# Kernel tuning notes

Hardware: AMD Instinct MI355X
Metric: run time of the kernel (lower is better)

Reference implementation:

```python
import jax, jax.numpy as jnp
import numpy as np
from jax import lax

L = 2        # encoder layers
D = 256      # d_model
H = 8        # nhead
DH = D // H  # head dim
CF = 2       # compression_factor (default in CustomizedAttn)
FF = 2048    # dim_feedforward
B = 10       # batch (forced: null_k has shape (10,1,D))
HH = 40
WW = 40
T = HH * WW  # seq len = 1600
EPS = 1e-5


def setup_inputs() -> dict:
    key = jax.random.key(0)
    ks = jax.random.split(key, 16)
    f = lambda k, shp: jax.random.normal(k, shp, jnp.float32) * 0.02
    return {
        "src": jax.random.normal(ks[0], (B, D, HH, WW), jnp.float32),
        "pos_embed": jax.random.normal(ks[1], (B, D, HH, WW), jnp.float32),
        "Wq": f(ks[2], (L, D, D)),
        "Wk": f(ks[3], (L, D, D)),
        "Wv": f(ks[4], (L, D, D)),
        "Wo": f(ks[5], (L, D, D)),
        "bo": jnp.zeros((L, D), jnp.float32),
        "conv_w": f(ks[6], (L, D, D // H, CF)),  # grouped Conv1d weight [out, in/groups, k]
        "conv_b": jnp.zeros((L, D), jnp.float32),
        "null_k": f(ks[7], (L, B, 1, D)),
        "null_v": f(ks[8], (L, B, 1, D)),
        "ln1_g": jnp.ones((L, D), jnp.float32),
        "ln1_b": jnp.zeros((L, D), jnp.float32),
        "ln2_g": jnp.ones((L, D), jnp.float32),
        "ln2_b": jnp.zeros((L, D), jnp.float32),
        "W1": f(ks[9], (L, FF, D)),
        "b1": jnp.zeros((L, FF), jnp.float32),
        "W2": f(ks[10], (L, D, FF)),
        "b2": jnp.zeros((L, D), jnp.float32),
    }


def _layernorm(x, g, b):
    m = jnp.mean(x, axis=-1, keepdims=True)
    v = jnp.var(x, axis=-1, keepdims=True)
    return (x - m) * lax.rsqrt(v + EPS) * g + b


def _attn(x, pos, Wq, Wk, Wv, Wo, bo, cw, cb, nk, nv):
    # x, pos: [B, T, D]
    qk = x + pos
    q = qk @ Wq.T
    k = qk @ Wk.T
    v = x @ Wv.T
    # torch: padding = cf - t % cf -> always in [1, cf], so padding ALWAYS applied
    pad = CF - (T % CF)
    k = jnp.pad(k, ((0, 0), (pad, 0), (0, 0)))
    v = jnp.pad(v, ((0, 0), (pad, 0), (0, 0)))

    def compress(t_):  # grouped strided Conv1d over time, shared weights for k and v
        y = lax.conv_general_dilated(
            t_.transpose(0, 2, 1), cw, (CF,), "VALID",
            dimension_numbers=("NCH", "OIH", "NCH"), feature_group_count=H)
        return (y + cb[None, :, None]).transpose(0, 2, 1)

    k = jnp.concatenate([nk, compress(k)], axis=1)  # [B, Tc+10, D]
    v = jnp.concatenate([nv, compress(v)], axis=1)
    split = lambda t_: t_.reshape(B, t_.shape[1], H, DH).transpose(0, 2, 1, 3)
    qh, kh, vh = split(q), split(k), split(v)
    # NOTE: scale uses FULL d_model (d ** -0.5), faithful to the source.
    dots = jnp.einsum("bhid,bhjd->bhij", qh, kh) * (D ** -0.5)
    # NOTE: the source computes softmax(dots) but then overwrites it with
    # dropout(dots); at inference attention weights are the raw scaled dots.
    out = jnp.einsum("bhij,bhjd->bhid", dots, vh)
    out = out.transpose(0, 2, 1, 3).reshape(B, T, D)
    return out @ Wo.T + bo


def reference(src, pos_embed, Wq, Wk, Wv, Wo, bo, conv_w, conv_b, null_k, null_v,
              ln1_g, ln1_b, ln2_g, ln2_b, W1, b1, W2, b2):
    x = src.reshape(B, D, T).transpose(0, 2, 1)        # [B, T, D]
    pos = pos_embed.reshape(B, D, T).transpose(0, 2, 1)
    for l in range(L):
        a = _attn(x, pos, Wq[l], Wk[l], Wv[l], Wo[l], bo[l],
                  conv_w[l], conv_b[l], null_k[l], null_v[l])
        x = _layernorm(x + a, ln1_g[l], ln1_b[l])
        ff = jnp.maximum(x @ W1[l].T + b1[l], 0.0) @ W2[l].T + b2[l]
        x = _layernorm(x + ff, ln2_g[l], ln2_b[l])
    return x.transpose(0, 2, 1).reshape(B, D, HH, WW)
```

## Files before the change

### kernel.cpp

```cpp
#include <hip/hip_runtime.h>
#include <math.h>

typedef __attribute__((ext_vector_type(8))) short short8;
typedef __attribute__((ext_vector_type(4))) short short4v;
typedef __attribute__((ext_vector_type(4))) float f32x4;
typedef unsigned int u32;

constexpr int Bsz = 10;
constexpr int Dm  = 256;
constexpr int Hh  = 8;
constexpr int Tt  = 1600;
constexpr int FFd = 2048;
constexpr int Tkv = 802;
constexpr int JCH = 8;
constexpr size_t Fsz  = (size_t)Bsz * Tt * Dm;
constexpr size_t PAD  = 65536;
constexpr size_t KVsz = (size_t)Bsz * Tkv * Dm;
constexpr size_t FHsz = (size_t)Bsz * Tt * FFd;
constexpr size_t WBsz = 2621440;

__device__ float g_x[Fsz];
__device__ float g_qk[Fsz];
__device__ float g_t[Fsz];
__device__ float g_kc[KVsz];
__device__ float g_vc[KVsz];
__device__ float g_kvm[(size_t)Bsz * Hh * 32 * 32];
__device__ float g_kvp[(size_t)JCH * Bsz * Hh * 32 * 32];
__device__ float g_pos[Fsz];
__device__ unsigned short g_xb[Fsz + PAD];
__device__ unsigned short g_qkb[Fsz + PAD];
__device__ unsigned short g_tb[Fsz + PAD];
__device__ unsigned short g_qb[Fsz + PAD];
__device__ unsigned short g_ffh[FHsz + PAD];
__device__ unsigned short g_wb[WBsz];
__device__ unsigned short g_wo2[(size_t)Bsz * Dm * Dm];

__device__ __forceinline__ float* selbuf(int id) {
  switch (id) {
    case 0: return g_x;
    case 1: return g_qk;
    case 2: return g_t;
    case 3: return g_kc;
    case 4: return g_vc;
    default: return g_kvm;
  }
}
__device__ __forceinline__ unsigned short* selbufb(int id) {
  switch (id) {
    case 0: return g_xb;
    case 1: return g_qkb;
    case 2: return g_tb;
    case 3: return g_ffh;
    default: return g_qb;
  }
}

__device__ __forceinline__ unsigned short f2b(float x) {
  unsigned int u = __float_as_uint(x);
  u += 0x7FFFu + ((u >> 16) & 1u);
  return (unsigned short)(u >> 16);
}
__device__ __forceinline__ float b2f(unsigned short u) {
  return __uint_as_float(((unsigned int)u) << 16);
}

__global__ __launch_bounds__(256) void wconv_k(const float* src, int dstoff, int n) {
  int i = blockIdx.x * 256 + threadIdx.x;
  if (i < n) g_wb[dstoff + i] = f2b(src[i]);
}

__global__ __launch_bounds__(256) void trans_in_k(const float* in, int oid) {
  __shared__ float tile[32][33];
  const int tx = threadIdx.x & 31, ty = threadIdx.x >> 5;
  const int t0 = blockIdx.x * 32, d0 = blockIdx.y * 32, b = blockIdx.z;
  #pragma unroll
  for (int i = ty; i < 32; i += 8)
    tile[i][tx] = in[((size_t)(b * Dm + d0 + i)) * Tt + t0 + tx];
  __syncthreads();
  float* out = (oid == 0) ? g_x : g_pos;
  #pragma unroll
  for (int i = ty; i < 32; i += 8) {
    const size_t idx = ((size_t)(b * Tt + t0 + i)) * Dm + d0 + tx;
    float v = tile[tx][i];
    out[idx] = v;
    if (oid == 0) g_xb[idx] = f2b(v);
  }
}

__global__ __launch_bounds__(256) void trans_out_k(float* out) {
  __shared__ float tile[32][33];
  const int tx = threadIdx.x & 31, ty = threadIdx.x >> 5;
  const int t0 = blockIdx.x * 32, d0 = blockIdx.y * 32, b = blockIdx.z;
  #pragma unroll
  for (int i = ty; i < 32; i += 8)
    tile[i][tx] = g_x[((size_t)(b * Tt + t0 + i)) * Dm + d0 + tx];
  __syncthreads();
  #pragma unroll
  for (int i = ty; i < 32; i += 8)
    out[((size_t)(b * Dm + d0 + i)) * Tt + t0 + tx] = tile[tx][i];
}

__global__ __launch_bounds__(256) void addpos_k(int n4) {
  int i = blockIdx.x * 256 + threadIdx.x;
  if (i >= n4) return;
  float4 a = ((const float4*)g_x)[i];
  float4 p = ((const float4*)g_pos)[i];
  short4v v;
  v[0] = (short)f2b(a.x + p.x); v[1] = (short)f2b(a.y + p.y);
  v[2] = (short)f2b(a.z + p.z); v[3] = (short)f2b(a.w + p.w);
  *(short4v*)&g_qkb[(size_t)i * 4] = v;
}

template<int BN, bool DUAL, bool PERB, bool RELU, bool BIAS, bool CBF16>
__global__ __launch_bounds__(256) void gemm2_k(
    int Aid, int woff, const float* __restrict__ bias, int Cid, int C2id,
    int NB, int M, int N, int K) {
  constexpr int BM = 128, BK = 64;
  constexpr int ACH = BM * 8;
  constexpr int BCH = BN * 8;
  constexpr int NW = BN / 32;
  __shared__ short8 As8[2][ACH];
  __shared__ short8 Bs8[2][BCH];
  const int tid = threadIdx.x;
  const int lane = tid & 63, wid = tid >> 6;
  const int wr = wid >> 1, wc = wid & 1;

  const int nwg = gridDim.x;
  const int bid = blockIdx.x;
  const int q = nwg >> 3, r = nwg & 7;
  const int xcd = bid & 7, seq = bid >> 3;
  const int wgid = (xcd < r ? xcd * (q + 1) : r * (q + 1) + (xcd - r) * q) + seq;

  int m0, n0, mlim;
  const unsigned short* W16;
  if constexpr (PERB) {
    const int per = 13 * NB;
    const int b = wgid / per;
    const int rem = wgid - b * per;
    m0 = b * Tt + (rem / NB) * BM;
    n0 = (rem % NB) * BN;
    mlim = b * Tt + Tt;
    W16 = g_wo2 + (size_t)b * 65536;
  } else {
    m0 = (wgid / NB) * BM;
    n0 = (wgid % NB) * BN;
    mlim = M;
    W16 = g_wb + woff;
  }

  const unsigned short* A16 = selbufb(Aid);
  const bool second = DUAL && (n0 >= 256);
  float* Cf = selbuf(second ? C2id : Cid);
  unsigned short* C16 = selbufb(second ? C2id : Cid);
  const int gn0 = second ? n0 - 256 : n0;
  const int cstride = DUAL ? 256 : N;

  f32x4 acc[4][NW];
  #pragma unroll
  for (int m = 0; m < 4; ++m)
    #pragma unroll
    for (int n = 0; n < NW; ++n) acc[m][n] = (f32x4){0.f, 0.f, 0.f, 0.f};

  const int lkc = lane >> 4, lrc = lane & 15;

  auto stage = [&](int t, int buf) {
    const int k0 = t * BK;
    #pragma unroll
    for (int i = 0; i < ACH / 256; ++i) {
      const int c = tid + i * 256;
      const int row = c >> 3, kc = c & 7;
      const unsigned short* gs = A16 + (size_t)(m0 + row) * K + k0 +
                                 ((kc ^ (row & 7)) << 3);
      __builtin_amdgcn_global_load_lds(
          (const __attribute__((address_space(1))) u32*)gs,
          (__attribute__((address_space(3))) u32*)&As8[buf][c], 16, 0, 0);
    }
    #pragma unroll
    for (int i = 0; i < BCH / 256; ++i) {
      const int c = tid + i * 256;
      const int row = c >> 3, kc = c & 7;
      const unsigned short* gs = W16 + (size_t)(n0 + row) * K + k0 +
                                 ((kc ^ (row & 7)) << 3);
      __builtin_amdgcn_global_load_lds(
          (const __attribute__((address_space(1))) u32*)gs,
          (__attribute__((address_space(3))) u32*)&Bs8[buf][c], 16, 0, 0);
    }
  };

  const int nt = K / BK;
  stage(0, 0);
  if (nt > 1) stage(1, 1);
  for (int t = 0; t < nt; ++t) {
    const int cur = t & 1;
    if (t + 1 < nt) {
      if constexpr (BN == 64)
        asm volatile("s_waitcnt vmcnt(6)" ::: "memory");
      else
        asm volatile("s_waitcnt vmcnt(8)" ::: "memory");
    } else {
      asm volatile("s_waitcnt vmcnt(0)" ::: "memory");
    }
    __builtin_amdgcn_sched_barrier(0);
    __builtin_amdgcn_s_barrier();
    #pragma unroll
    for (int kk = 0; kk < 2; ++kk) {
      short8 af[4], bf[NW];
      #pragma unroll
      for (int m = 0; m < 4; ++m) {
        const int r2 = wr * 64 + m * 16 + lrc;
        af[m] = As8[cur][r2 * 8 + ((kk * 4 + lkc) ^ (r2 & 7))];
      }
      #pragma unroll
      for (int n = 0; n < NW; ++n) {
        const int cn = wc * (BN / 2) + n * 16 + lrc;
        bf[n] = Bs8[cur][cn * 8 + ((kk * 4 + lkc) ^ (cn & 7))];
      }
      #pragma unroll
      for (int m = 0; m < 4; ++m)
        #pragma unroll
        for (int n = 0; n < NW; ++n)
          acc[m][n] = __builtin_amdgcn_mfma_f32_16x16x32_bf16(
              af[m], bf[n], acc[m][n], 0, 0, 0);
    }
    __builtin_amdgcn_sched_barrier(0);
    __builtin_amdgcn_s_barrier();
    __builtin_amdgcn_sched_barrier(0);
    if (t + 2 < nt) stage(t + 2, cur);
  }

  constexpr int CSTR = (BN == 64) ? BN + 4 : BN;
  float* ldsC = (float*)&As8[0][0];
  {
    asm volatile("s_waitcnt vmcnt(0)" ::: "memory");
    __builtin_amdgcn_s_barrier();
    const int r0 = lkc * 4;
    #pragma unroll
    for (int m = 0; m < 4; ++m)
      #pragma unroll
      for (int n = 0; n < NW; ++n) {
        const int col = wc * (BN / 2) + n * 16 + lrc;
        #pragma unroll
        for (int j = 0; j < 4; ++j)
          ldsC[(wr * 64 + m * 16 + r0 + j) * CSTR + col] = acc[m][n][j];
      }
    __syncthreads();
  }
  if constexpr (CBF16) {
    constexpr int CH = BM * BN / 8;
    #pragma unroll
    for (int i = 0; i < CH / 256; ++i) {
      const int c = tid + i * 256;
      const int rowl = c / (BN / 8), col8 = (c % (BN / 8)) * 8;
      if (PERB && m0 + rowl >= mlim) continue;
      short8 v;
      #pragma unroll
      for (int j = 0; j < 8; ++j) {
        float x = ldsC[rowl * CSTR + col8 + j];
        if (BIAS) x += bias[gn0 + col8 + j];
        if (RELU) x = fmaxf(x, 0.f);
        v[j] = (short)f2b(x);
      }
      *(short8*)(C16 + (size_t)(m0 + rowl) * cstride + gn0 + col8) = v;
    }
  } else {
    constexpr int CH = BM * BN / 4;
    #pragma unroll
    for (int i = 0; i < CH / 256; ++i) {
      const int c = tid + i * 256;
      const int rowl = c / (BN / 4), col4 = (c % (BN / 4)) * 4;
      if (PERB && m0 + rowl >= mlim) continue;
      float4 v;
      float* pv = &v.x;
      #pragma unroll
      for (int j = 0; j < 4; ++j) {
        float x = ldsC[rowl * CSTR + col4 + j];
        if (BIAS) x += bias[gn0 + col4 + j];
        if (RELU) x = fmaxf(x, 0.f);
        pv[j] = x;
      }
      *(float4*)(Cf + (size_t)(m0 + rowl) * cstride + gn0 + col4) = v;
    }
  }
}

template<bool RELU, bool BIAS, bool CBF16>
__global__ __launch_bounds__(512, 4) void gemmh_k(
    int Aid, int woff, const float* __restrict__ bias, int Cid,
    int NB, int M, int N) {
  constexpr int BM = 128, BN = 128, K = 256, KH = 128;
  __shared__ short8 As8[BM * 16];
  __shared__ short8 Bs8[BN * 16];
  const int tid = threadIdx.x;
  const int lane = tid & 63, wid = tid >> 6;
  const int wr = wid >> 2, wc = wid & 3;
  const int nwg = gridDim.x;
  const int bid = blockIdx.x;
  const int q = nwg >> 3, r = nwg & 7;
  const int xcd = bid & 7, seq = bid >> 3;
  const int wgid = (xcd < r ? xcd * (q + 1) : r * (q + 1) + (xcd - r) * q) + seq;
  const int m0 = (wgid / NB) * BM, n0 = (wgid % NB) * BN;
  const unsigned short* A16 = selbufb(Aid);
  const unsigned short* W16 = g_wb + woff;
  float* Cf = selbuf(Cid);
  unsigned short* C16 = selbufb(Cid);
  const int lkc = lane >> 4, lrc = lane & 15;

  f32x4 acc[4][2];
  #pragma unroll
  for (int m = 0; m < 4; ++m)
    #pragma unroll
    for (int n = 0; n < 2; ++n) acc[m][n] = (f32x4){0.f, 0.f, 0.f, 0.f};

  #pragma unroll
  for (int h = 0; h < 2; ++h) {
    const int k0 = h * KH;
    if (h) __builtin_amdgcn_s_barrier();
    #pragma unroll
    for (int i = 0; i < (BM * 16) / 512; ++i) {
      const int c = tid + i * 512;
      const int row = c >> 4, kc = c & 15;
      const unsigned short* gs = A16 + (size_t)(m0 + row) * K + k0 +
                                 ((kc ^ (row & 15)) << 3);
      __builtin_amdgcn_global_load_lds(
          (const __attribute__((address_space(1))) u32*)gs,
          (__attribute__((address_space(3))) u32*)&As8[c], 16, 0, 0);
    }
    #pragma unroll
    for (int i = 0; i < (BN * 16) / 512; ++i) {
      const int c = tid + i * 512;
      const int row = c >> 4, kc = c & 15;
      const unsigned short* gs = W16 + (size_t)(n0 + row) * K + k0 +
                                 ((kc ^ (row & 15)) << 3);
      __builtin_amdgcn_global_load_lds(
          (const __attribute__((address_space(1))) u32*)gs,
          (__attribute__((address_space(3))) u32*)&Bs8[c], 16, 0, 0);
    }
    asm volatile("s_waitcnt vmcnt(0)" ::: "memory");
    __builtin_amdgcn_sched_barrier(0);
    __builtin_amdgcn_s_barrier();

    __builtin_amdgcn_s_setprio(1);
    #pragma unroll
    for (int s = 0; s < 4; ++s) {
      short8 af[4], bf[2];
      #pragma unroll
      for (int m = 0; m < 4; ++m) {
        const int r2 = wr * 64 + m * 16 + lrc;
        af[m] = As8[r2 * 16 + ((s * 4 + lkc) ^ (r2 & 15))];
      }
      #pragma unroll
      for (int n = 0; n < 2; ++n) {
        const int cn = wc * 32 + n * 16 + lrc;
        bf[n] = Bs8[cn * 16 + ((s * 4 + lkc) ^ (cn & 15))];
      }
      #pragma unroll
      for (int m = 0; m < 4; ++m)
        #pragma unroll
        for (int n = 0; n < 2; ++n)
          acc[m][n] = __builtin_amdgcn_mfma_f32_16x16x32_bf16(
              af[m], bf[n], acc[m][n], 0, 0, 0);
    }
    __builtin_amdgcn_s_setprio(0);
  }

  const int r0 = lkc * 4;
  #pragma unroll
  for (int m = 0; m < 4; ++m) {
    const int gmb = m0 + wr * 64 + m * 16 + r0;
    #pragma unroll
    for (int n = 0; n < 2; ++n) {
      const int gn = n0 + wc * 32 + n * 16 + lrc;
      const float bb = BIAS ? bias[gn] : 0.f;
      #pragma unroll
      for (int j = 0; j < 4; ++j) {
        float v = acc[m][n][j] + bb;
        if (RELU) v = fmaxf(v, 0.f);
        if (CBF16) C16[(size_t)(gmb + j) * N + gn] = f2b(v);
        else       Cf[(size_t)(gmb + j) * N + gn] = v;
      }
    }
  }
}

__global__ __launch_bounds__(256) void compress_main_k(
    const float* __restrict__ cw, const float* __restrict__ cb,
    const float* __restrict__ nul, int out_id) {
  __shared__ float rows[32][256];
  const int tc0 = 1 + blockIdx.x * 16;
  const int b = blockIdx.y;
  const int tid = threadIdx.x;
  const int o = tid;
  const int g = o >> 5;

  const int r0g = 2 * tc0 - 2;
  const unsigned short* src = g_tb + ((size_t)b * Tt + r0g) * Dm;
  #pragma unroll
  for (int i = 0; i < 4; ++i) {
    const int c = tid + i * 256;
    const int row = c >> 5, off = (c & 31) * 8;
    short8 v = *(const short8*)(src + (size_t)row * 256 + off);
    #pragma unroll
    for (int j = 0; j < 8; ++j)
      rows[row][off + j] = b2f((unsigned short)v[j]);
  }

  float we[32], wo[32];
  {
    const float4* wp = (const float4*)(cw + o * 64);
    #pragma unroll
    for (int i = 0; i < 16; ++i) {
      float4 w4 = wp[i];
      we[i * 2 + 0] = w4.x; wo[i * 2 + 0] = w4.y;
      we[i * 2 + 1] = w4.z; wo[i * 2 + 1] = w4.w;
    }
  }
  const float bias = cb[o];
  float* outb = selbuf(out_id) + (size_t)b * Tkv * Dm;
  if (blockIdx.x == 0) {
    outb[o] = nul[b * Dm + o];
    outb[Dm + o] = bias;
  }
  __syncthreads();

  float* outp = outb + o;
  #pragma unroll
  for (int t = 0; t < 16; ++t) {
    const int lr = 2 * t;
    const float* p0 = &rows[lr][g * 32];
    const float* p1 = &rows[lr + 1][g * 32];
    float acc = bias;
    #pragma unroll
    for (int i4 = 0; i4 < 8; ++i4) {
      float4 a0 = *(const float4*)(p0 + i4 * 4);
      float4 a1 = *(const float4*)(p1 + i4 * 4);
      acc = fmaf(we[i4 * 4 + 0], a0.x, acc);
      acc = fmaf(we[i4 * 4 + 1], a0.y, acc);
      acc = fmaf(we[i4 * 4 + 2], a0.z, acc);
      acc = fmaf(we[i4 * 4 + 3], a0.w, acc);
      acc = fmaf(wo[i4 * 4 + 0], a1.x, acc);
      acc = fmaf(wo[i4 * 4 + 1], a1.y, acc);
      acc = fmaf(wo[i4 * 4 + 2], a1.z, acc);
      acc = fmaf(wo[i4 * 4 + 3], a1.w, acc);
    }
    outp[(size_t)(1 + tc0 + t) * Dm] = acc;
  }
}

__global__ __launch_bounds__(256) void kvout1_k() {
  __shared__ float kl[8][32];
  __shared__ float vl[8][32];
  const int bh = blockIdx.x;
  const int js = blockIdx.y;
  const int b = bh >> 3, h = bh & 7;
  const int j0 = js * 101;
  const int jend = (j0 + 101 < Tkv) ? j0 + 101 : Tkv;

  const int tid = threadIdx.x;
  const int lr = tid >> 5;
  const int lc = tid & 31;
  const int e = tid >> 3;
  const int d0 = (tid & 7) * 4;

  float a0 = 0.f, a1 = 0.f, a2 = 0.f, a3 = 0.f;
  const size_t base = (size_t)b * Tkv * Dm + h * 32;

  for (int jc = j0; jc < jend; jc += 8) {
    const int jr = jc + lr;
    if (jr < jend) {
      kl[lr][lc] = g_kc[base + (size_t)jr * Dm + lc];
      vl[lr][lc] = g_vc[base + (size_t)jr * Dm + lc];
    } else {
      kl[lr][lc] = 0.f;
      vl[lr][lc] = 0.f;
    }
    __syncthreads();
    #pragma unroll
    for (int r = 0; r < 8; ++r) {
      const float kf = kl[r][e];
      const float* vr = &vl[r][d0];
      a0 = fmaf(kf, vr[0], a0);
      a1 = fmaf(kf, vr[1], a1);
      a2 = fmaf(kf, vr[2], a2);
      a3 = fmaf(kf, vr[3], a3);
    }
    __syncthreads();
  }
  float* op = g_kvp + ((size_t)js * 80 + bh) * 1024 + e * 32 + d0;
  op[0] = a0; op[1] = a1; op[2] = a2; op[3] = a3;
}

__global__ __launch_bounds__(256) void kvout2_k() {
  const int bh = blockIdx.x;
  const int tid = threadIdx.x;
  const int e = tid >> 3;
  const int d0 = (tid & 7) * 4;
  float a0 = 0.f, a1 = 0.f, a2 = 0.f, a3 = 0.f;
  #pragma unroll
  for (int s = 0; s < JCH; ++s) {
    const float* p = g_kvp + ((size_t)s * 80 + bh) * 1024 + e * 32 + d0;
    a0 += p[0]; a1 += p[1]; a2 += p[2]; a3 += p[3];
  }
  float* op = g_kvm + (size_t)bh * 1024 + e * 32 + d0;
  op[0] = a0 * 0.0625f;
  op[1] = a1 * 0.0625f;
  op[2] = a2 * 0.0625f;
  op[3] = a3 * 0.0625f;
}

__global__ __launch_bounds__(256) void wo2_k(int wooff) {
  const int n = blockIdx.x, b = blockIdx.y;
  const int he = threadIdx.x;
  const int h = he >> 5, e = he & 31;
  const float* kp = g_kvm + ((size_t)(b * Hh + h) * 32 + e) * 32;
  const unsigned short* wp = g_wb + wooff + (size_t)n * Dm + h * 32;
  float acc = 0.f;
  #pragma unroll
  for (int d = 0; d < 32; ++d) acc = fmaf(kp[d], b2f(wp[d]), acc);
  g_wo2[(size_t)b * 65536 + (size_t)n * Dm + he] = f2b(acc);
}

__global__ __launch_bounds__(256) void ln_k(int did, const float* g,
                                            const float* beta, int do_pos) {
  const int lane = threadIdx.x & 63;
  const int wave = threadIdx.x >> 6;
  const size_t row = (size_t)blockIdx.x * 4 + wave;
  float4 xv = ((const float4*)g_x)[row * 64 + lane];
  float4 dv = ((const float4*)selbuf(did))[row * 64 + lane];
  float v[4] = {xv.x + dv.x, xv.y + dv.y, xv.z + dv.z, xv.w + dv.w};
  float sum = v[0] + v[1] + v[2] + v[3];
  float sq = v[0]*v[0] + v[1]*v[1] + v[2]*v[2] + v[3]*v[3];
  #pragma unroll
  for (int off = 32; off; off >>= 1) {
    sum += __shfl_xor(sum, off);
    sq  += __shfl_xor(sq, off);
  }
  const float mean = sum * (1.f / 256.f);
  const float var = sq * (1.f / 256.f) - mean * mean;
  const float rs = rsqrtf(var + 1e-5f);
  float4 gg = ((const float4*)g)[lane];
  float4 bb = ((const float4*)beta)[lane];
  float4 ov;
  ov.x = (v[0] - mean) * rs * gg.x + bb.x;
  ov.y = (v[1] - mean) * rs * gg.y + bb.y;
  ov.z = (v[2] - mean) * rs * gg.z + bb.z;
  ov.w = (v[3] - mean) * rs * gg.w + bb.w;
  ((float4*)g_x)[row * 64 + lane] = ov;
  short4v sv;
  sv[0] = (short)f2b(ov.x); sv[1] = (short)f2b(ov.y);
  sv[2] = (short)f2b(ov.z); sv[3] = (short)f2b(ov.w);
  *(short4v*)&g_xb[(row * 64 + lane) * 4] = sv;
  if (do_pos) {
    float4 pv = ((const float4*)g_pos)[row * 64 + lane];
    short4v qv;
    qv[0] = (short)f2b(ov.x + pv.x); qv[1] = (short)f2b(ov.y + pv.y);
    qv[2] = (short)f2b(ov.z + pv.z); qv[3] = (short)f2b(ov.w + pv.w);
    *(short4v*)&g_qkb[(row * 64 + lane) * 4] = qv;
  }
}

extern "C" void kernel_launch(void* const* d_in, const int* in_sizes, int n_in,
                              void* d_out, int out_size, void* d_ws, size_t ws_size,
                              hipStream_t stream) {
  const float* src  = (const float*)d_in[0];
  const float* pose = (const float*)d_in[1];
  const float* Wq   = (const float*)d_in[2];
  const float* Wk   = (const float*)d_in[3];
  const float* Wv   = (const float*)d_in[4];
  const float* Wo   = (const float*)d_in[5];
  const float* bo   = (const float*)d_in[6];
  const float* cw   = (const float*)d_in[7];
  const float* cb   = (const float*)d_in[8];
  const float* nk   = (const float*)d_in[9];
  const float* nv   = (const float*)d_in[10];
  const float* ln1g = (const float*)d_in[11];
  const float* ln1b = (const float*)d_in[12];
  const float* ln2g = (const float*)d_in[13];
  const float* ln2b = (const float*)d_in[14];
  const float* W1   = (const float*)d_in[15];
  const float* b1   = (const float*)d_in[16];
  const float* W2   = (const float*)d_in[17];
  const float* b2   = (const float*)d_in[18];

  const int MT = Bsz * Tt;
  const int NF = (int)Fsz;
  const dim3 tgrid(Tt / 32, Dm / 32, Bsz);

  const int OV = 262144, OO = 393216, O1 = 524288, O2 = 1572864;
  for (int l = 0; l < 2; ++l) {
    wconv_k<<<256, 256, 0, stream>>>(Wk + (size_t)l * 65536, l * 131072, 65536);
    wconv_k<<<256, 256, 0, stream>>>(Wq + (size_t)l * 65536, l * 131072 + 65536, 65536);
    wconv_k<<<256, 256, 0, stream>>>(Wv + (size_t)l * 65536, OV + l * 65536, 65536);
    wconv_k<<<256, 256, 0, stream>>>(Wo + (size_t)l * 65536, OO + l * 65536, 65536);
  }
  wconv_k<<<4096, 256, 0, stream>>>(W1, O1, 1048576);
  wconv_k<<<4096, 256, 0, stream>>>(W2, O2, 1048576);

  trans_in_k<<<tgrid, 256, 0, stream>>>(src, 0);
  trans_in_k<<<tgrid, 256, 0, stream>>>(pose, 7);

  const int MB = MT / 128;
  for (int l = 0; l < 2; ++l) {
    const float* bo_l = bo + (size_t)l * Dm;
    const float* cw_l = cw + (size_t)l * Dm * 64;
    const float* cb_l = cb + (size_t)l * Dm;
    const float* nk_l = nk + (size_t)l * Bsz * Dm;
    const float* nv_l = nv + (size_t)l * Bsz * Dm;
    const float* b1_l = b1 + (size_t)l * FFd;
    const float* b2_l = b2 + (size_t)l * Dm;
    const int wkq = l * 131072;
    const int wv = OV + l * 65536, wo = OO + l * 65536;
    const int w1 = O1 + l * 524288, w2 = O2 + l * 524288;

    if (l == 0) addpos_k<<<NF / 4 / 256, 256, 0, stream>>>(NF / 4);
    gemm2_k<64, true, false, false, false, true><<<8 * MB, 256, 0, stream>>>(
        1, wkq, nullptr, 2, 4, 8, MT, 512, Dm);
    compress_main_k<<<dim3(50, Bsz), 256, 0, stream>>>(cw_l, cb_l, nk_l, 3);
    gemm2_k<64, false, false, false, false, true><<<4 * MB, 256, 0, stream>>>(
        0, wv, nullptr, 2, 2, 4, MT, Dm, Dm);
    compress_main_k<<<dim3(50, Bsz), 256, 0, stream>>>(cw_l, cb_l, nv_l, 4);
    kvout1_k<<<dim3(Bsz * Hh, JCH), 256, 0, stream>>>();
    kvout2_k<<<Bsz * Hh, 256, 0, stream>>>();
    wo2_k<<<dim3(Dm, Bsz), 256, 0, stream>>>(wo);
    gemm2_k<64, false, true, false, true, false><<<Bsz * 13 * 4, 256, 0, stream>>>(
        4, 0, bo_l, 2, 2, 4, MT, Dm, Dm);
    ln_k<<<MT / 4, 256, 0, stream>>>(2, ln1g + l * Dm, ln1b + l * Dm, 0);

    gemmh_k<true, true, true><<<16 * MB, 512, 0, stream>>>(
        0, w1, b1_l, 3, 16, MT, FFd);
    gemm2_k<64, false, false, false, true, false><<<4 * MB, 256, 0, stream>>>(
        3, w2, b2_l, 1, 1, 4, MT, Dm, FFd);
    ln_k<<<MT / 4, 256, 0, stream>>>(1, ln2g + l * Dm, ln2b + l * Dm,
                                     l == 0 ? 1 : 0);
  }

  trans_out_k<<<tgrid, 256, 0, stream>>>((float*)d_out);
}
```

Before: 409.4 us.

## Fuse setup kernels, merge compress launches, add split-K W2 GEMM

Merges the ten weight-conversion launches into one kernel, fuses the two input transposes with the pos-add and bf16 casts, and batches the K and V compression into a single launch by writing V to a separate buffer. The W2 feed-forward GEMM is replaced by a new split-K kernel with a 128x256 tile. It writes its two partial sums to separate buffers, and the following layernorm now reads and adds both. This is meant to cut launch overhead and improve occupancy on the K=2048 GEMM, at the cost of an extra fp32 partial buffer round-trip through memory.

New measurement: 385.2 us. 1.06x faster.

```diff
diff --git a/kernel.cpp b/kernel.cpp
--- a/kernel.cpp
+++ b/kernel.cpp
@@ -64,26 +64,48 @@
   return __uint_as_float(((unsigned int)u) << 16);
 }
 
-__global__ __launch_bounds__(256) void wconv_k(const float* src, int dstoff, int n) {
-  int i = blockIdx.x * 256 + threadIdx.x;
-  if (i < n) g_wb[dstoff + i] = f2b(src[i]);
-}
-
-__global__ __launch_bounds__(256) void trans_in_k(const float* in, int oid) {
-  __shared__ float tile[32][33];
+__global__ __launch_bounds__(256) void wconv_all_k(
+    const float* __restrict__ Wk, const float* __restrict__ Wq,
+    const float* __restrict__ Wv, const float* __restrict__ Wo,
+    const float* __restrict__ W1, const float* __restrict__ W2) {
+  const int i = blockIdx.x * 256 + threadIdx.x;
+  float v;
+  if (i < 262144) {
+    const int l = i >> 17, r = i & 131071;
+    v = (r < 65536) ? Wk[l * 65536 + r] : Wq[l * 65536 + (r - 65536)];
+  } else if (i < 393216) {
+    v = Wv[i - 262144];
+  } else if (i < 524288) {
+    v = Wo[i - 393216];
+  } else if (i < 1572864) {
+    v = W1[i - 524288];
+  } else {
+    v = W2[i - 1572864];
+  }
+  g_wb[i] = f2b(v);
+}
+
+__global__ __launch_bounds__(256) void trans_in2_k(const float* __restrict__ src,
+                                                   const float* __restrict__ pose) {
+  __shared__ float ts[32][33];
+  __shared__ float tp[32][33];
   const int tx = threadIdx.x & 31, ty = threadIdx.x >> 5;
   const int t0 = blockIdx.x * 32, d0 = blockIdx.y * 32, b = blockIdx.z;
   #pragma unroll
-  for (int i = ty; i < 32; i += 8)
-    tile[i][tx] = in[((size_t)(b * Dm + d0 + i)) * Tt + t0 + tx];
+  for (int i = ty; i < 32; i += 8) {
+    const size_t gi = ((size_t)(b * Dm + d0 + i)) * Tt + t0 + tx;
+    ts[i][tx] = src[gi];
+    tp[i][tx] = pose[gi];
+  }
   __syncthreads();
-  float* out = (oid == 0) ? g_x : g_pos;
   #pragma unroll
   for (int i = ty; i < 32; i += 8) {
     const size_t idx = ((size_t)(b * Tt + t0 + i)) * Dm + d0 + tx;
-    float v = tile[tx][i];
-    out[idx] = v;
-    if (oid == 0) g_xb[idx] = f2b(v);
+    const float s = ts[tx][i], p = tp[tx][i];
+    g_x[idx] = s;
+    g_pos[idx] = p;
+    g_xb[idx] = f2b(s);
+    g_qkb[idx] = f2b(s + p);
   }
 }
 
@@ -98,17 +120,6 @@
   #pragma unroll
   for (int i = ty; i < 32; i += 8)
     out[((size_t)(b * Dm + d0 + i)) * Tt + t0 + tx] = tile[tx][i];
-}
-
-__global__ __launch_bounds__(256) void addpos_k(int n4) {
-  int i = blockIdx.x * 256 + threadIdx.x;
-  if (i >= n4) return;
-  float4 a = ((const float4*)g_x)[i];
-  float4 p = ((const float4*)g_pos)[i];
-  short4v v;
-  v[0] = (short)f2b(a.x + p.x); v[1] = (short)f2b(a.y + p.y);
-  v[2] = (short)f2b(a.z + p.z); v[3] = (short)f2b(a.w + p.w);
-  *(short4v*)&g_qkb[(size_t)i * 4] = v;
 }
 
 template<int BN, bool DUAL, bool PERB, bool RELU, bool BIAS, bool CBF16>
@@ -279,6 +290,110 @@
         pv[j] = x;
       }
       *(float4*)(Cf + (size_t)(m0 + rowl) * cstride + gn0 + col4) = v;
+    }
+  }
+}
+
+__global__ __launch_bounds__(512, 2) void gemmn_k(
+    int Aid, int woff, const float* __restrict__ bias, int K) {
+  constexpr int BM = 128, BN = 256, BK = 64;
+  constexpr int ACH = BM * 8;
+  constexpr int BCH = BN * 8;
+  __shared__ short8 As8[2][ACH];
+  __shared__ short8 Bs8[2][BCH];
+  const int tid = threadIdx.x;
+  const int lane = tid & 63, wid = tid >> 6;
+  const int wr = wid >> 2, wc = wid & 3;
+  const int nwg = gridDim.x, bid = blockIdx.x;
+  const int q = nwg >> 3, r = nwg & 7;
+  const int xcd = bid & 7, seq = bid >> 3;
+  const int wgid = (xcd < r ? xcd * (q + 1) : r * (q + 1) + (xcd - r) * q) + seq;
+  const int half = nwg >> 1;
+  const int ks = (wgid >= half) ? 1 : 0;
+  const int m0 = (wgid - ks * half) * BM;
+  const int kbase = ks * (K >> 1);
+  const unsigned short* A16 = selbufb(Aid);
+  const unsigned short* W16 = g_wb + woff;
+  float* Cf = ks ? g_t : g_qk;
+
+  f32x4 acc[4][4];
+  #pragma unroll
+  for (int m = 0; m < 4; ++m)
+    #pragma unroll
+    for (int n = 0; n < 4; ++n) acc[m][n] = (f32x4){0.f, 0.f, 0.f, 0.f};
+
+  const int lkc = lane >> 4, lrc = lane & 15;
+
+  auto stage = [&](int t, int buf) {
+    const int k0 = kbase + t * BK;
+    #pragma unroll
+    for (int i = 0; i < ACH / 512; ++i) {
+      const int c = tid + i * 512;
+      const int row = c >> 3, kc = c & 7;
+      const unsigned short* gs = A16 + (size_t)(m0 + row) * K + k0 +
+                                 ((kc ^ (row & 7)) << 3);
+      __builtin_amdgcn_global_load_lds(
+          (const __attribute__((address_space(1))) u32*)gs,
+          (__attribute__((address_space(3))) u32*)&As8[buf][c], 16, 0, 0);
+    }
+    #pragma unroll
+    for (int i = 0; i < BCH / 512; ++i) {
+      const int c = tid + i * 512;
+      const int row = c >> 3, kc = c & 7;
+      const unsigned short* gs = W16 + (size_t)row * K + k0 +
+                                 ((kc ^ (row & 7)) << 3);
+      __builtin_amdgcn_global_load_lds(
+          (const __attribute__((address_space(1))) u32*)gs,
+          (__attribute__((address_space(3))) u32*)&Bs8[buf][c], 16, 0, 0);
+    }
+  };
+
+  const int nt = (K >> 1) / BK;
+  stage(0, 0);
+  stage(1, 1);
+  for (int t = 0; t < nt; ++t) {
+    const int cur = t & 1;
+    if (t + 1 < nt) asm volatile("s_waitcnt vmcnt(6)" ::: "memory");
+    else            asm volatile("s_waitcnt vmcnt(0)" ::: "memory");
+    __builtin_amdgcn_sched_barrier(0);
+    __builtin_amdgcn_s_barrier();
+    #pragma unroll
+    for (int kk = 0; kk < 2; ++kk) {
+      short8 af[4], bf[4];
+      #pragma unroll
+      for (int m = 0; m < 4; ++m) {
+        const int r2 = wr * 64 + m * 16 + lrc;
+        af[m] = As8[cur][r2 * 8 + ((kk * 4 + lkc) ^ (r2 & 7))];
+      }
+      #pragma unroll
+      for (int n = 0; n < 4; ++n) {
+        const int cn = wc * 64 + n * 16 + lrc;
+        bf[n] = Bs8[cur][cn * 8 + ((kk * 4 + lkc) ^ (cn & 7))];
+      }
+      #pragma unroll
+      for (int m = 0; m < 4; ++m)
+        #pragma unroll
+        for (int n = 0; n < 4; ++n)
+          acc[m][n] = __builtin_amdgcn_mfma_f32_16x16x32_bf16(
+              af[m], bf[n], acc[m][n], 0, 0, 0);
+    }
+    __builtin_amdgcn_sched_barrier(0);
+    __builtin_amdgcn_s_barrier();
+    __builtin_amdgcn_sched_barrier(0);
+    if (t + 2 < nt) stage(t + 2, cur);
+  }
+
+  const int r0 = lkc * 4;
+  #pragma unroll
+  for (int m = 0; m < 4; ++m) {
+    const int gm = m0 + wr * 64 + m * 16 + r0;
+    #pragma unroll
+    for (int n = 0; n < 4; ++n) {
+      const int gn = wc * 64 + n * 16 + lrc;
+      const float bb = (ks == 0) ? bias[gn] : 0.f;
+      #pragma unroll
+      for (int j = 0; j < 4; ++j)
+        Cf[(size_t)(gm + j) * BN + gn] = acc[m][n][j] + bb;
     }
   }
 }
@@ -382,18 +497,23 @@
   }
 }
 
-__global__ __launch_bounds__(256) void compress_main_k(
+__global__ __launch_bounds__(256) void compress2_k(
     const float* __restrict__ cw, const float* __restrict__ cb,
-    const float* __restrict__ nul, int out_id) {
+    const float* __restrict__ nk, const float* __restrict__ nv) {
   __shared__ float rows[32][256];
   const int tc0 = 1 + blockIdx.x * 16;
   const int b = blockIdx.y;
+  const int z = blockIdx.z;
   const int tid = threadIdx.x;
   const int o = tid;
   const int g = o >> 5;
 
+  const unsigned short* srcbuf = z ? g_ffh : g_tb;
+  const float* nul = z ? nv : nk;
+  float* outb = (z ? g_vc : g_kc) + (size_t)b * Tkv * Dm;
+
   const int r0g = 2 * tc0 - 2;
-  const unsigned short* src = g_tb + ((size_t)b * Tt + r0g) * Dm;
+  const unsigned short* src = srcbuf + ((size_t)b * Tt + r0g) * Dm;
   #pragma unroll
   for (int i = 0; i < 4; ++i) {
     const int c = tid + i * 256;
@@ -415,7 +535,6 @@
     }
   }
   const float bias = cb[o];
-  float* outb = selbuf(out_id) + (size_t)b * Tkv * Dm;
   if (blockIdx.x == 0) {
     outb[o] = nul[b * Dm + o];
     outb[Dm + o] = bias;
@@ -519,7 +638,7 @@
   g_wo2[(size_t)b * 65536 + (size_t)n * Dm + he] = f2b(acc);
 }
 
-__global__ __launch_bounds__(256) void ln_k(int did, const float* g,
+__global__ __launch_bounds__(256) void ln_k(int did, int did2, const float* g,
                                             const float* beta, int do_pos) {
   const int lane = threadIdx.x & 63;
   const int wave = threadIdx.x >> 6;
@@ -527,6 +646,10 @@
   float4 xv = ((const float4*)g_x)[row * 64 + lane];
   float4 dv = ((const float4*)selbuf(did))[row * 64 + lane];
   float v[4] = {xv.x + dv.x, xv.y + dv.y, xv.z + dv.z, xv.w + dv.w};
+  if (did2 >= 0) {
+    float4 d2 = ((const float4*)selbuf(did2))[row * 64 + lane];
+    v[0] += d2.x; v[1] += d2.y; v[2] += d2.z; v[3] += d2.w;
+  }
   float sum = v[0] + v[1] + v[2] + v[3];
   float sq = v[0]*v[0] + v[1]*v[1] + v[2]*v[2] + v[3]*v[3];
   #pragma unroll
@@ -582,21 +705,11 @@
   const float* b2   = (const float*)d_in[18];
 
   const int MT = Bsz * Tt;
-  const int NF = (int)Fsz;
   const dim3 tgrid(Tt / 32, Dm / 32, Bsz);
 
   const int OV = 262144, OO = 393216, O1 = 524288, O2 = 1572864;
-  for (int l = 0; l < 2; ++l) {
-    wconv_k<<<256, 256, 0, stream>>>(Wk + (size_t)l * 65536, l * 131072, 65536);
-    wconv_k<<<256, 256, 0, stream>>>(Wq + (size_t)l * 65536, l * 131072 + 65536, 65536);
-    wconv_k<<<256, 256, 0, stream>>>(Wv + (size_t)l * 65536, OV + l * 65536, 65536);
-    wconv_k<<<256, 256, 0, stream>>>(Wo + (size_t)l * 65536, OO + l * 65536, 65536);
-  }
-  wconv_k<<<4096, 256, 0, stream>>>(W1, O1, 1048576);
-  wconv_k<<<4096, 256, 0, stream>>>(W2, O2, 1048576);
-
-  trans_in_k<<<tgrid, 256, 0, stream>>>(src, 0);
-  trans_in_k<<<tgrid, 256, 0, stream>>>(pose, 7);
+  wconv_all_k<<<10240, 256, 0, stream>>>(Wk, Wq, Wv, Wo, W1, W2);
+  trans_in2_k<<<tgrid, 256, 0, stream>>>(src, pose);
 
   const int MB = MT / 128;
   for (int l = 0; l < 2; ++l) {
@@ -611,25 +724,22 @@
     const int wv = OV + l * 65536, wo = OO + l * 65536;
     const int w1 = O1 + l * 524288, w2 = O2 + l * 524288;
 
-    if (l == 0) addpos_k<<<NF / 4 / 256, 256, 0, stream>>>(NF / 4);
     gemm2_k<64, true, false, false, false, true><<<8 * MB, 256, 0, stream>>>(
         1, wkq, nullptr, 2, 4, 8, MT, 512, Dm);
-    compress_main_k<<<dim3(50, Bsz), 256, 0, stream>>>(cw_l, cb_l, nk_l, 3);
     gemm2_k<64, false, false, false, false, true><<<4 * MB, 256, 0, stream>>>(
-        0, wv, nullptr, 2, 2, 4, MT, Dm, Dm);
-    compress_main_k<<<dim3(50, Bsz), 256, 0, stream>>>(cw_l, cb_l, nv_l, 4);
+        0, wv, nullptr, 3, 3, 4, MT, Dm, Dm);
+    compress2_k<<<dim3(50, Bsz, 2), 256, 0, stream>>>(cw_l, cb_l, nk_l, nv_l);
     kvout1_k<<<dim3(Bsz * Hh, JCH), 256, 0, stream>>>();
     kvout2_k<<<Bsz * Hh, 256, 0, stream>>>();
     wo2_k<<<dim3(Dm, Bsz), 256, 0, stream>>>(wo);
     gemm2_k<64, false, true, false, true, false><<<Bsz * 13 * 4, 256, 0, stream>>>(
         4, 0, bo_l, 2, 2, 4, MT, Dm, Dm);
-    ln_k<<<MT / 4, 256, 0, stream>>>(2, ln1g + l * Dm, ln1b + l * Dm, 0);
+    ln_k<<<MT / 4, 256, 0, stream>>>(2, -1, ln1g + l * Dm, ln1b + l * Dm, 0);
 
     gemmh_k<true, true, true><<<16 * MB, 512, 0, stream>>>(
         0, w1, b1_l, 3, 16, MT, FFd);
-    gemm2_k<64, false, false, false, true, false><<<4 * MB, 256, 0, stream>>>(
-        3, w2, b2_l, 1, 1, 4, MT, Dm, FFd);
-    ln_k<<<MT / 4, 256, 0, stream>>>(1, ln2g + l * Dm, ln2b + l * Dm,
+    gemmn_k<<<2 * MB, 512, 0, stream>>>(3, w2, b2_l, FFd);
+    ln_k<<<MT / 4, 256, 0, stream>>>(1, 2, ln2g + l * Dm, ln2b + l * Dm,
                                      l == 0 ? 1 : 0);
   }
 
```
